# Kernel tuning notes

Measured on AMD Instinct MI355X. Metric: run time of the kernel, lower is better.

The kernel has to match this reference:

```python
import jax, jax.numpy as jnp
import numpy as np

N = 50000   # nodes
E = 800000  # edges
IN, H, OUT = 64, 512, 128


def _lin_init(key, out_dim, in_dim):
    kw, kb = jax.random.split(key)
    bound = 1.0 / np.sqrt(in_dim)
    W = jax.random.uniform(kw, (out_dim, in_dim), jnp.float32, -bound, bound)
    b = jax.random.uniform(kb, (out_dim,), jnp.float32, -bound, bound)
    return W, b


def setup_inputs() -> dict:
    key = jax.random.key(0)
    ks = jax.random.split(key, 10)
    x = jax.random.normal(ks[0], (N, IN), jnp.float32)
    edge_index = jax.random.randint(ks[1], (2, E), 0, N, jnp.int64)
    W_s1, b_s1 = _lin_init(ks[2], H, IN)
    W_s2, b_s2 = _lin_init(ks[3], H, H)
    W_s3, b_s3 = _lin_init(ks[4], H, H)
    W_s4, b_s4 = _lin_init(ks[5], H, H)
    W_m1, b_m1 = _lin_init(ks[6], OUT, H)
    W_m2, b_m2 = _lin_init(ks[7], OUT, OUT)
    W_l1, b_l1 = _lin_init(ks[8], OUT, H)
    W_l2, b_l2 = _lin_init(ks[9], OUT, OUT)
    return {"x": x, "edge_index": edge_index,
            "W_s1": W_s1, "b_s1": b_s1, "W_s2": W_s2, "b_s2": b_s2,
            "W_s3": W_s3, "b_s3": b_s3, "W_s4": W_s4, "b_s4": b_s4,
            "W_m1": W_m1, "b_m1": b_m1, "W_m2": W_m2, "b_m2": b_m2,
            "W_l1": W_l1, "b_l1": b_l1, "W_l2": W_l2, "b_l2": b_l2}


def _aggregate(h, src, dst):
    # GINConv with default eps=0: (1+eps)*x + sum_{j in N(i)} x_j
    return h + jax.ops.segment_sum(h[src], dst, num_segments=N)


def reference(x, edge_index,
              W_s1, b_s1, W_s2, b_s2, W_s3, b_s3, W_s4, b_s4,
              W_m1, b_m1, W_m2, b_m2, W_l1, b_l1, W_l2, b_l2):
    src, dst = edge_index[0], edge_index[1]
    lrelu = lambda v: jax.nn.leaky_relu(v, 0.1)

    def mlp_shared(h):
        h = lrelu(h @ W_s1.T + b_s1)
        h = lrelu(h @ W_s2.T + b_s2)
        h = lrelu(h @ W_s3.T + b_s3)
        return h @ W_s4.T + b_s4

    def mlp_mu(h):
        return jax.nn.relu(h @ W_m1.T + b_m1) @ W_m2.T + b_m2

    def mlp_logvar(h):
        return jax.nn.relu(h @ W_l1.T + b_l1) @ W_l2.T + b_l2

    h = jax.nn.relu(mlp_shared(_aggregate(x, src, dst)))
    mu = mlp_mu(_aggregate(h, src, dst))
    logvar = mlp_logvar(_aggregate(h, src, dst))
    return (mu, logvar)
```

## Files before the change

kernel.cpp:

```cpp
#include <hip/hip_runtime.h>
#include <hip/hip_bf16.h>
#include <stdint.h>

#define N_NODES 50000
#define N_PAD   50048
#define E_EDGES 800000
#define MT      391

typedef __bf16 bf16x8 __attribute__((ext_vector_type(8)));
typedef __bf16 bf16x4 __attribute__((ext_vector_type(4)));
typedef float  f32x4  __attribute__((ext_vector_type(4)));

__global__ void count_deg(const int* __restrict__ ei, int* __restrict__ cnt) {
    int e = blockIdx.x * blockDim.x + threadIdx.x;
    if (e < E_EDGES) atomicAdd(&cnt[ei[E_EDGES + e]], 1);
}

#define SCAN_B 1024
__global__ void scan_block(const int* __restrict__ cnt, int* __restrict__ ptr,
                           int* __restrict__ bsum, int n) {
    __shared__ int buf[SCAN_B];
    int i = blockIdx.x * SCAN_B + threadIdx.x;
    int v = (i < n) ? cnt[i] : 0;
    buf[threadIdx.x] = v;
    __syncthreads();
    #pragma unroll
    for (int off = 1; off < SCAN_B; off <<= 1) {
        int t = (threadIdx.x >= (unsigned)off) ? buf[threadIdx.x - off] : 0;
        __syncthreads();
        buf[threadIdx.x] += t;
        __syncthreads();
    }
    if (i < n) ptr[i] = buf[threadIdx.x] - v;
    if (threadIdx.x == SCAN_B - 1) bsum[blockIdx.x] = buf[SCAN_B - 1];
}

__global__ void scan_bsums(const int* __restrict__ bsum, int* __restrict__ boff,
                           int nb, int* __restrict__ total_out) {
    __shared__ int buf[SCAN_B];
    int v = ((int)threadIdx.x < nb) ? bsum[threadIdx.x] : 0;
    buf[threadIdx.x] = v;
    __syncthreads();
    #pragma unroll
    for (int off = 1; off < SCAN_B; off <<= 1) {
        int t = (threadIdx.x >= (unsigned)off) ? buf[threadIdx.x - off] : 0;
        __syncthreads();
        buf[threadIdx.x] += t;
        __syncthreads();
    }
    if ((int)threadIdx.x < nb) boff[threadIdx.x] = buf[threadIdx.x] - v;
    if (threadIdx.x == SCAN_B - 1) *total_out = buf[SCAN_B - 1];
}

__global__ void scan_add(int* __restrict__ ptr, const int* __restrict__ boff, int n) {
    int i = blockIdx.x * SCAN_B + threadIdx.x;
    if (i < n) ptr[i] += boff[blockIdx.x];
}

__global__ void fill_csr(const int* __restrict__ ei, const int* __restrict__ ptr,
                         int* __restrict__ cursor, int* __restrict__ col) {
    int e = blockIdx.x * blockDim.x + threadIdx.x;
    if (e < E_EDGES) {
        int dst = ei[E_EDGES + e];
        int pos = ptr[dst] + atomicAdd(&cursor[dst], 1);
        col[pos] = ei[e];
    }
}

#define XN      3200000
#define WTOT    983040
__global__ void cvt_all(const float* __restrict__ x,
                        const float* __restrict__ Ws1, const float* __restrict__ Ws2,
                        const float* __restrict__ Ws3, const float* __restrict__ Ws4,
                        const float* __restrict__ Wm1, const float* __restrict__ Wl1,
                        const float* __restrict__ Wm2, const float* __restrict__ Wl2,
                        __bf16* __restrict__ xb, __bf16* __restrict__ wbuf) {
    int i = blockIdx.x * blockDim.x + threadIdx.x;
    if (i < XN) { xb[i] = (__bf16)x[i]; return; }
    int j = i - XN;
    if (j >= WTOT) return;
    const float* s; int o;
    if      (j <  32768) { s = Ws1; o = j; }
    else if (j < 294912) { s = Ws2; o = j -  32768; }
    else if (j < 557056) { s = Ws3; o = j - 294912; }
    else if (j < 819200) { s = Ws4; o = j - 557056; }
    else if (j < 884736) { s = Wm1; o = j - 819200; }
    else if (j < 950272) { s = Wl1; o = j - 884736; }
    else if (j < 966656) { s = Wm2; o = j - 950272; }
    else                 { s = Wl2; o = j - 966656; }
    wbuf[j] = (__bf16)s[o];
}

__global__ __launch_bounds__(256) void agg0_gather(
    const __bf16* __restrict__ xb, const int* __restrict__ ptr,
    const int* __restrict__ col, __bf16* __restrict__ out) {
    int node = blockIdx.x * 4 + (threadIdx.x >> 6);
    int lane = threadIdx.x & 63;
    int g    = lane >> 3;
    int f0   = (lane & 7) << 3;
    if (node >= N_PAD) return;
    long o = (long)node * 64 + f0;
    if (node >= N_NODES) {
        if (g == 0) {
            bf16x8 z;
            #pragma unroll
            for (int i = 0; i < 8; ++i) z[i] = (__bf16)0.0f;
            *(bf16x8*)&out[o] = z;
        }
        return;
    }
    float a[8];
    #pragma unroll
    for (int i = 0; i < 8; ++i) a[i] = 0.0f;
    if (g == 0) {
        bf16x8 s = *(const bf16x8*)&xb[o];
        #pragma unroll
        for (int i = 0; i < 8; ++i) a[i] = (float)s[i];
    }
    int e0 = ptr[node], e1 = ptr[node + 1];
    int e = e0;
    for (; e + 16 <= e1; e += 16) {
        int c0 = col[e + g];
        int c1 = col[e + 8 + g];
        bf16x8 v0 = *(const bf16x8*)&xb[(c0 << 6) + f0];
        bf16x8 v1 = *(const bf16x8*)&xb[(c1 << 6) + f0];
        #pragma unroll
        for (int i = 0; i < 8; ++i) a[i] += (float)v0[i] + (float)v1[i];
    }
    int rem = e1 - e;
    if (rem > 0) {
        int u0 = (g < rem) ? g : 0;        float m0 = (g < rem) ? 1.0f : 0.0f;
        int i1 = g + 8;
        int u1 = (i1 < rem) ? i1 : 0;      float m1 = (i1 < rem) ? 1.0f : 0.0f;
        int c0 = col[e + u0];
        int c1 = col[e + u1];
        bf16x8 v0 = *(const bf16x8*)&xb[(c0 << 6) + f0];
        bf16x8 v1 = *(const bf16x8*)&xb[(c1 << 6) + f0];
        #pragma unroll
        for (int i = 0; i < 8; ++i) a[i] += m0 * (float)v0[i] + m1 * (float)v1[i];
    }
    #pragma unroll
    for (int i = 0; i < 8; ++i) {
        a[i] += __shfl_xor(a[i], 8, 64);
        a[i] += __shfl_xor(a[i], 16, 64);
        a[i] += __shfl_xor(a[i], 32, 64);
    }
    if (g == 0) {
        bf16x8 r;
        #pragma unroll
        for (int i = 0; i < 8; ++i) r[i] = (__bf16)a[i];
        *(bf16x8*)&out[o] = r;
    }
}

__global__ __launch_bounds__(256) void aggt_gather(
    const __bf16* __restrict__ t, const int* __restrict__ ptr,
    const int* __restrict__ col, const float* __restrict__ b_m1,
    const float* __restrict__ b_l1, __bf16* __restrict__ p) {
    int node = blockIdx.x * 8 + (threadIdx.x >> 5);
    if (node >= N_NODES) return;
    int hl = threadIdx.x & 31;
    int f0 = hl << 3;
    float a[8];
    {
        bf16x8 s = *(const bf16x8*)&t[((long)node << 8) + f0];
        #pragma unroll
        for (int i = 0; i < 8; ++i) a[i] = (float)s[i];
    }
    int e0 = ptr[node], e1 = ptr[node + 1];
    int e = e0;
    for (; e + 8 <= e1; e += 8) {
        int c[8];
        #pragma unroll
        for (int u = 0; u < 8; ++u) c[u] = col[e + u];
        bf16x8 v[8];
        #pragma unroll
        for (int u = 0; u < 8; ++u) v[u] = *(const bf16x8*)&t[((long)c[u] << 8) + f0];
        #pragma unroll
        for (int u = 0; u < 8; ++u)
            #pragma unroll
            for (int i = 0; i < 8; ++i) a[i] += (float)v[u][i];
    }
    int rem = e1 - e;
    if (rem > 0) {
        #pragma unroll
        for (int u = 0; u < 7; ++u) {
            int   uu = (u < rem) ? u : 0;
            float m  = (u < rem) ? 1.0f : 0.0f;
            int   cc = col[e + uu];
            bf16x8 v = *(const bf16x8*)&t[((long)cc << 8) + f0];
            #pragma unroll
            for (int i = 0; i < 8; ++i) a[i] += m * (float)v[i];
        }
    }
    const float* bp = (f0 < 128) ? (b_m1 + f0) : (b_l1 + (f0 - 128));
    f32x4 b0 = *(const f32x4*)bp;
    f32x4 b1 = *(const f32x4*)(bp + 4);
    bf16x8 r;
    #pragma unroll
    for (int i = 0; i < 4; ++i) r[i]     = (__bf16)fmaxf(a[i]     + b0[i], 0.0f);
    #pragma unroll
    for (int i = 0; i < 4; ++i) r[4 + i] = (__bf16)fmaxf(a[4 + i] + b1[i], 0.0f);
    *(bf16x8*)&p[((long)node << 8) + f0] = r;
}

__device__ __forceinline__ void gl_lds16(const __bf16* g, __bf16* l) {
    __builtin_amdgcn_global_load_lds(
        (const __attribute__((address_space(1))) uint32_t*)g,
        (__attribute__((address_space(3))) uint32_t*)l, 16, 0, 0);
}

#define P_WAITN(n) asm volatile("s_waitcnt vmcnt(" #n ")" ::: "memory")
#define P_LGKM0 asm volatile("s_waitcnt lgkmcnt(0)" ::: "memory")
#define P_BAR   __builtin_amdgcn_s_barrier()

__device__ __forceinline__ void stage_chunk(const __bf16* __restrict__ W, int Kdim,
                                            int k0, bool rows512,
                                            __bf16* __restrict__ buf,
                                            int wid, int lane) {
    if (rows512) {
        int r16 = lane >> 2, sl = lane & 3;
        #pragma unroll
        for (int i = 0; i < 4; ++i) {
            int cc = wid * 4 + i;
            int r  = cc * 16 + r16;
            int kt = sl ^ ((r >> 1) & 3);
            gl_lds16(W + (long)r * Kdim + k0 + kt * 8, buf + cc * 512);
        }
    } else {
        int r8 = lane >> 3, sl = lane & 7;
        #pragma unroll
        for (int i = 0; i < 4; ++i) {
            int cc = wid * 4 + i;
            int r  = cc * 8 + r8;
            int kt = sl ^ (r & 7);
            gl_lds16(W + (long)r * Kdim + k0 + kt * 8, buf + cc * 512);
        }
    }
}

__device__ __forceinline__ void chunk_mfma4(const __bf16* __restrict__ sAct,
    const __bf16* __restrict__ buf, int c, int rA, int q, int wncol,
    f32x4 (&acc)[4][4]) {
    const int g   = c * 4 + q;
    const int sla = ((g & 56) | ((g & 7) ^ (rA & 7))) << 3;
    bf16x8 af[4], bfr[4];
    #pragma unroll
    for (int mi = 0; mi < 4; ++mi)
        af[mi] = *(const bf16x8*)&sAct[(mi * 16 + rA) * 512 + sla];
    #pragma unroll
    for (int ni = 0; ni < 4; ++ni) {
        int wr = wncol + ni * 16 + rA;
        bfr[ni] = *(const bf16x8*)&buf[wr * 32 + ((q ^ ((wr >> 1) & 3)) << 3)];
    }
    #pragma unroll
    for (int mi = 0; mi < 4; ++mi)
        #pragma unroll
        for (int ni = 0; ni < 4; ++ni)
            acc[mi][ni] = __builtin_amdgcn_mfma_f32_16x16x32_bf16(
                af[mi], bfr[ni], acc[mi][ni], 0, 0, 0);
}

__device__ __forceinline__ void chunk_mfma_a0(const __bf16* __restrict__ act0,
    const __bf16* __restrict__ buf, int c, int rA, int q, int wncol,
    f32x4 (&acc)[4][4]) {
    const int g   = c * 4 + q;
    const int sla = (g ^ (rA & 7)) << 3;
    bf16x8 af[4], bfr[4];
    #pragma unroll
    for (int mi = 0; mi < 4; ++mi)
        af[mi] = *(const bf16x8*)&act0[(mi * 16 + rA) * 64 + sla];
    #pragma unroll
    for (int ni = 0; ni < 4; ++ni) {
        int wr = wncol + ni * 16 + rA;
        bfr[ni] = *(const bf16x8*)&buf[wr * 32 + ((q ^ ((wr >> 1) & 3)) << 3)];
    }
    #pragma unroll
    for (int mi = 0; mi < 4; ++mi)
        #pragma unroll
        for (int ni = 0; ni < 4; ++ni)
            acc[mi][ni] = __builtin_amdgcn_mfma_f32_16x16x32_bf16(
                af[mi], bfr[ni], acc[mi][ni], 0, 0, 0);
}

__device__ __forceinline__ void chunk_mfma_proj(const __bf16* __restrict__ sAct,
    const __bf16* __restrict__ buf, int c, int rA, int q, int wnp,
    f32x4 (&accp)[4][2]) {
    #pragma unroll
    for (int s = 0; s < 2; ++s) {
        const int g   = c * 8 + s * 4 + q;
        const int sla = ((g & 56) | ((g & 7) ^ (rA & 7))) << 3;
        bf16x8 af[4], bfr[2];
        #pragma unroll
        for (int mi = 0; mi < 4; ++mi)
            af[mi] = *(const bf16x8*)&sAct[(mi * 16 + rA) * 512 + sla];
        #pragma unroll
        for (int ni = 0; ni < 2; ++ni) {
            int wr = wnp + ni * 16 + rA;
            int gB = s * 4 + q;
            bfr[ni] = *(const bf16x8*)&buf[wr * 64 + ((gB ^ (wr & 7)) << 3)];
        }
        #pragma unroll
        for (int mi = 0; mi < 4; ++mi)
            #pragma unroll
            for (int ni = 0; ni < 2; ++ni)
                accp[mi][ni] = __builtin_amdgcn_mfma_f32_16x16x32_bf16(
                    af[mi], bfr[ni], accp[mi][ni], 0, 0, 0);
    }
}

template <int ACTn>
__device__ __forceinline__ void writeback_act(__bf16* __restrict__ sAct,
    f32x4 (&acc)[4][4], const float* __restrict__ bv,
    int wn, int ccol, int crow) {
    #pragma unroll
    for (int mi = 0; mi < 4; ++mi)
        #pragma unroll
        for (int ni = 0; ni < 4; ++ni) {
            int cc = wn + ni * 16 + ccol;
            int g  = cc >> 3;
            #pragma unroll
            for (int p = 0; p < 4; ++p) {
                int rr = mi * 16 + crow + p;
                float v = acc[mi][ni][p] + bv[ni];
                if (ACTn == 1) v = (v > 0.0f) ? v : 0.1f * v;
                else           v = fmaxf(v, 0.0f);
                int sl = (g & 56) | ((g & 7) ^ (rr & 7));
                sAct[rr * 512 + sl * 8 + (cc & 7)] = (__bf16)v;
            }
        }
}

template <int ACTn>
__device__ __forceinline__ void layer512_pipe(
    __bf16* __restrict__ sAct, __bf16* __restrict__ s0, __bf16* __restrict__ s1,
    const __bf16* __restrict__ W,
    const __bf16* __restrict__ Wn, int Kn, bool n512, int k0n_c1,
    const float* __restrict__ bv,
    int wn, int rA, int q, int ccol, int crow, int wid, int lane) {
    f32x4 acc[4][4];
    #pragma unroll
    for (int i = 0; i < 4; ++i)
        #pragma unroll
        for (int j = 0; j < 4; ++j) acc[i][j] = (f32x4)0.0f;
    #pragma unroll
    for (int c = 0; c < 16; ++c) {
        __bf16* cur = (c & 1) ? s1 : s0;
        P_WAITN(4); P_BAR;
        chunk_mfma4(sAct, cur, c, rA, q, wn, acc);
        if (c < 15) {
            P_LGKM0; P_BAR;
            if (c <= 13) stage_chunk(W, 512, (c + 2) * 32, true, cur, wid, lane);
            else         stage_chunk(Wn, Kn, 0, n512, s0, wid, lane);
        } else {
            P_LGKM0; P_BAR;
            writeback_act<ACTn>(sAct, acc, bv, wn, ccol, crow);
            __syncthreads();
            stage_chunk(Wn, Kn, k0n_c1, n512, s1, wid, lane);
        }
    }
}

__global__ __launch_bounds__(512) void mlp_fused(
    const __bf16* __restrict__ a0,
    const __bf16* __restrict__ w1, const float* __restrict__ b1,
    const __bf16* __restrict__ w2, const float* __restrict__ b2,
    const __bf16* __restrict__ w3, const float* __restrict__ b3,
    const __bf16* __restrict__ w4, const float* __restrict__ b4,
    const __bf16* __restrict__ wp,
    __bf16* __restrict__ tg)
{
    __shared__ __bf16 lds[69632];
    __bf16* act0 = lds;
    __bf16* sAct = lds + 4096;
    __bf16* s0   = lds + 36864;
    __bf16* s1   = lds + 53248;

    const int tid  = threadIdx.x;
    const int wid  = tid >> 6;
    const int lane = tid & 63;
    const long blockRow = (long)blockIdx.x * 64;

    const int rA   = lane & 15;
    const int q    = lane >> 4;
    const int ccol = lane & 15;
    const int crow = (lane >> 4) << 2;
    const int wn   = wid << 6;
    const int wnp  = wid << 5;

    float bv1[4], bv2[4], bv3[4], bv4[4];
    #pragma unroll
    for (int ni = 0; ni < 4; ++ni) {
        int idx = wn + ni * 16 + ccol;
        bv1[ni] = b1[idx]; bv2[ni] = b2[idx]; bv3[ni] = b3[idx]; bv4[ni] = b4[idx];
    }

    {
        int srow = lane >> 3;
        int skg  = (lane & 7) ^ srow;
        gl_lds16(a0 + (blockRow + wid * 8 + srow) * 64 + skg * 8, act0 + wid * 512);
    }
    stage_chunk(w1, 64, 0,  true, s0, wid, lane);
    stage_chunk(w1, 64, 32, true, s1, wid, lane);

    {
        f32x4 acc[4][4];
        #pragma unroll
        for (int i = 0; i < 4; ++i)
            #pragma unroll
            for (int j = 0; j < 4; ++j) acc[i][j] = (f32x4)0.0f;
        P_WAITN(4); P_BAR;
        chunk_mfma_a0(act0, s0, 0, rA, q, wn, acc);
        P_LGKM0; P_BAR;
        stage_chunk(w2, 512, 0, true, s0, wid, lane);
        P_WAITN(4); P_BAR;
        chunk_mfma_a0(act0, s1, 1, rA, q, wn, acc);
        writeback_act<1>(sAct, acc, bv1, wn, ccol, crow);
        __syncthreads();
        stage_chunk(w2, 512, 32, true, s1, wid, lane);
    }

    layer512_pipe<1>(sAct, s0, s1, w2, w3, 512, true, 32, bv2, wn, rA, q, ccol, crow, wid, lane);
    layer512_pipe<1>(sAct, s0, s1, w3, w4, 512, true, 32, bv3, wn, rA, q, ccol, crow, wid, lane);
    layer512_pipe<2>(sAct, s0, s1, w4, wp, 512, false, 64, bv4, wn, rA, q, ccol, crow, wid, lane);

    {
        f32x4 accp[4][2];
        #pragma unroll
        for (int i = 0; i < 4; ++i)
            #pragma unroll
            for (int j = 0; j < 2; ++j) accp[i][j] = (f32x4)0.0f;
        #pragma unroll
        for (int c = 0; c < 8; ++c) {
            __bf16* cur = (c & 1) ? s1 : s0;
            if (c == 7) { P_WAITN(0); } else { P_WAITN(4); }
            P_BAR;
            chunk_mfma_proj(sAct, cur, c, rA, q, wnp, accp);
            P_LGKM0; P_BAR;
            if (c < 6) stage_chunk(wp, 512, (c + 2) * 64, false, cur, wid, lane);
        }
        #pragma unroll
        for (int mi = 0; mi < 4; ++mi)
            #pragma unroll
            for (int ni = 0; ni < 2; ++ni)
                #pragma unroll
                for (int p = 0; p < 4; ++p)
                    s0[(mi * 16 + crow + p) * 256 + wnp + ni * 16 + ccol] =
                        (__bf16)accp[mi][ni][p];
        __syncthreads();
        int rr = tid >> 3;
        int c0 = (tid & 7) << 5;
        const bf16x8* s = (const bf16x8*)&s0[rr * 256 + c0];
        __bf16* d = tg + (blockRow + rr) * 256 + c0;
        #pragma unroll
        for (int i = 0; i < 4; ++i) *(bf16x8*)(d + i * 8) = s[i];
    }
}

template <int NCOL>
__device__ __forceinline__ void swizzle_xy(int bid, int& x, int& y) {
    int grp  = bid / (8 * NCOL);
    int rem  = bid - grp * (8 * NCOL);
    int base = grp * 8;
    int width = MT - base; if (width > 8) width = 8;
    x = base + rem % width;
    y = rem / width;
}

template <int ACT, bool BIAS, bool OUT_BF16, bool MCHK>
__device__ __forceinline__ void gemm_core(
    const __bf16* __restrict__ A, int lda, const __bf16* __restrict__ W,
    const float* __restrict__ bias, void* __restrict__ Cout, int ldc,
    int K, long Mstore, long blockRow, int blockCol,
    __bf16* __restrict__ smem) {
    __bf16* As = smem;
    __bf16* Ws = smem + 8192;
    const int tid  = threadIdx.x;
    const int wid  = tid >> 6;
    const int lane = tid & 63;
    const int wm = (wid >> 1) << 6;
    const int wn = (wid & 1) << 6;

    f32x4 acc[4][4];
    #pragma unroll
    for (int i = 0; i < 4; ++i)
        #pragma unroll
        for (int j = 0; j < 4; ++j) acc[i][j] = (f32x4)0.0f;

    const int srow = lane >> 3;
    const int skg  = (lane & 7) ^ srow;
    const __bf16* gA[4]; const __bf16* gW[4];
    __bf16 *lA[4], *lW[4];
    #pragma unroll
    for (int i = 0; i < 4; ++i) {
        int c = wid * 4 + i;
        gA[i] = A + (blockRow + c * 8 + srow) * (long)lda + skg * 8;
        gW[i] = W + ((long)blockCol + c * 8 + srow) * (long)K + skg * 8;
        lA[i] = As + c * 512;
        lW[i] = Ws + c * 512;
    }

    const int rA = lane & 15;
    const int q  = lane >> 4;
    const int r7 = rA & 7;

    for (int k0 = 0; k0 < K; k0 += 64) {
        #pragma unroll
        for (int i = 0; i < 4; ++i) gl_lds16(gA[i] + k0, lA[i]);
        #pragma unroll
        for (int i = 0; i < 4; ++i) gl_lds16(gW[i] + k0, lW[i]);
        __syncthreads();

        #pragma unroll
        for (int s = 0; s < 2; ++s) {
            const int slot = ((s * 4 + q) ^ r7) * 8;
            bf16x8 af[4], bf[4];
            #pragma unroll
            for (int mi = 0; mi < 4; ++mi)
                af[mi] = *(const bf16x8*)&As[(wm + mi * 16 + rA) * 64 + slot];
            #pragma unroll
            for (int ni = 0; ni < 4; ++ni)
                bf[ni] = *(const bf16x8*)&Ws[(wn + ni * 16 + rA) * 64 + slot];
            #pragma unroll
            for (int mi = 0; mi < 4; ++mi)
                #pragma unroll
                for (int ni = 0; ni < 4; ++ni)
                    acc[mi][ni] = __builtin_amdgcn_mfma_f32_16x16x32_bf16(
                        af[mi], bf[ni], acc[mi][ni], 0, 0, 0);
        }
        __syncthreads();
    }

    const int ccol = lane & 15;
    const int crow = (lane >> 4) << 2;
    if (OUT_BF16 && !MCHK) {
        #pragma unroll
        for (int mi = 0; mi < 4; ++mi) {
            #pragma unroll
            for (int ni = 0; ni < 4; ++ni) {
                int gc = wn + ni * 16 + ccol;
                float bv = BIAS ? bias[blockCol + gc] : 0.0f;
                #pragma unroll
                for (int r = 0; r < 4; ++r) {
                    float v = acc[mi][ni][r] + bv;
                    if (ACT == 1) v = (v > 0.0f) ? v : 0.1f * v;
                    else if (ACT == 2) v = fmaxf(v, 0.0f);
                    smem[(wm + mi * 16 + crow + r) * 128 + gc] = (__bf16)v;
                }
            }
        }
        __syncthreads();
        #pragma unroll
        for (int i = 0; i < 8; ++i) {
            int o   = (i * 256 + tid) * 8;
            int row = o >> 7;
            int co  = o & 127;
            *(bf16x8*)((__bf16*)Cout + (blockRow + row) * (long)ldc + blockCol + co) =
                *(const bf16x8*)&smem[o];
        }
    } else if (!OUT_BF16) {
        float* fsmem = (float*)smem;
        #pragma unroll
        for (int half = 0; half < 2; ++half) {
            __syncthreads();
            if ((wm >> 6) == half) {
                #pragma unroll
                for (int mi = 0; mi < 4; ++mi) {
                    #pragma unroll
                    for (int ni = 0; ni < 4; ++ni) {
                        int gc = wn + ni * 16 + ccol;
                        float bv = BIAS ? bias[blockCol + gc] : 0.0f;
                        #pragma unroll
                        for (int r = 0; r < 4; ++r) {
                            float v = acc[mi][ni][r] + bv;
                            if (ACT == 1) v = (v > 0.0f) ? v : 0.1f * v;
                            else if (ACT == 2) v = fmaxf(v, 0.0f);
                            fsmem[(mi * 16 + crow + r) * 128 + gc] = v;
                        }
                    }
                }
            }
            __syncthreads();
            #pragma unroll
            for (int i = 0; i < 8; ++i) {
                int o   = i * 256 + tid;
                int row = o >> 5;
                int co  = (o & 31) * 4;
                long gr = blockRow + half * 64 + row;
                if (!MCHK || gr < Mstore)
                    *(f32x4*)((float*)Cout + gr * (long)ldc + blockCol + co) =
                        *(const f32x4*)&fsmem[o * 4];
            }
        }
    } else {
        #pragma unroll
        for (int mi = 0; mi < 4; ++mi) {
            #pragma unroll
            for (int ni = 0; ni < 4; ++ni) {
                long gr0 = blockRow + wm + mi * 16 + crow;
                int  gc  = blockCol + wn + ni * 16 + ccol;
                float bv = BIAS ? bias[gc] : 0.0f;
                #pragma unroll
                for (int r = 0; r < 4; ++r) {
                    long gr = gr0 + r;
                    if (!MCHK || gr < Mstore) {
                        float v = acc[mi][ni][r] + bv;
                        if (ACT == 1) v = (v > 0.0f) ? v : 0.1f * v;
                        else if (ACT == 2) v = fmaxf(v, 0.0f);
                        ((__bf16*)Cout)[gr * ldc + gc] = (__bf16)v;
                    }
                }
            }
        }
    }
}

__global__ __launch_bounds__(256) void gemm_heads(
    const __bf16* __restrict__ p, const __bf16* __restrict__ wm2,
    const float* __restrict__ b_m2, float* __restrict__ mu,
    const __bf16* __restrict__ wl2, const float* __restrict__ b_l2,
    float* __restrict__ lv) {
    __shared__ __bf16 smem[128 * 128];
    int x, hd;
    swizzle_xy<2>(blockIdx.x, x, hd);
    if (hd == 0)
        gemm_core<0, true, false, true>(p, 256, wm2, b_m2, mu, 128, 128, N_NODES,
                                        (long)x * 128, 0, smem);
    else
        gemm_core<0, true, false, true>(p + 128, 256, wl2, b_l2, lv, 128, 128, N_NODES,
                                        (long)x * 128, 0, smem);
}

extern "C" void kernel_launch(void* const* d_in, const int* in_sizes, int n_in,
                              void* d_out, int out_size, void* d_ws, size_t ws_size,
                              hipStream_t stream) {
    const float* x    = (const float*)d_in[0];
    const int*   ei   = (const int*)d_in[1];
    const float* W_s1 = (const float*)d_in[2];
    const float* b_s1 = (const float*)d_in[3];
    const float* W_s2 = (const float*)d_in[4];
    const float* b_s2 = (const float*)d_in[5];
    const float* W_s3 = (const float*)d_in[6];
    const float* b_s3 = (const float*)d_in[7];
    const float* W_s4 = (const float*)d_in[8];
    const float* b_s4 = (const float*)d_in[9];
    const float* W_m1 = (const float*)d_in[10];
    const float* b_m1 = (const float*)d_in[11];
    const float* W_m2 = (const float*)d_in[12];
    const float* b_m2 = (const float*)d_in[13];
    const float* W_l1 = (const float*)d_in[14];
    const float* b_l1 = (const float*)d_in[15];
    const float* W_l2 = (const float*)d_in[16];
    const float* b_l2 = (const float*)d_in[17];

    char* ws = (char*)d_ws;
    size_t off = 0;
    auto carve = [&](size_t bytes) -> void* {
        void* p = ws + off;
        off = (off + bytes + 255) & ~(size_t)255;
        return p;
    };
    int* ptr  = (int*)carve((size_t)(N_NODES + 1) * 4);
    int* col  = (int*)carve((size_t)E_EDGES * 4);
    int* bsum = (int*)carve(SCAN_B * 4);
    int* boff = (int*)carve(SCAN_B * 4);
    __bf16* wbuf = (__bf16*)carve((size_t)WTOT * 2);
    __bf16* w1  = wbuf;
    __bf16* w2  = wbuf +  32768;
    __bf16* w3  = wbuf + 294912;
    __bf16* w4  = wbuf + 557056;
    __bf16* wml = wbuf + 819200;
    __bf16* wm2 = wbuf + 950272;
    __bf16* wl2 = wbuf + 966656;
    __bf16* xb    = (__bf16*)carve((size_t)XN * 2);
    __bf16* agg0b = (__bf16*)carve((size_t)N_PAD * 64 * 2);
    __bf16* B1    = (__bf16*)carve((size_t)N_PAD * 512 * 2);
    __bf16* B2    = (__bf16*)carve((size_t)N_PAD * 512 * 2);

    int* cnt = (int*)B1;
    int* cur = (int*)B2;

    (void)hipMemsetAsync(cnt, 0, (size_t)N_NODES * 4, stream);
    (void)hipMemsetAsync(cur, 0, (size_t)N_NODES * 4, stream);

    const int NB = (N_NODES + SCAN_B - 1) / SCAN_B;
    count_deg<<<E_EDGES / 256, 256, 0, stream>>>(ei, cnt);
    scan_block<<<NB, SCAN_B, 0, stream>>>(cnt, ptr, bsum, N_NODES);
    scan_bsums<<<1, SCAN_B, 0, stream>>>(bsum, boff, NB, &ptr[N_NODES]);
    scan_add<<<NB, SCAN_B, 0, stream>>>(ptr, boff, N_NODES);
    fill_csr<<<E_EDGES / 256, 256, 0, stream>>>(ei, ptr, cur, col);

    cvt_all<<<(XN + WTOT + 255) / 256, 256, 0, stream>>>(
        x, W_s1, W_s2, W_s3, W_s4, W_m1, W_l1, W_m2, W_l2, xb, wbuf);

    agg0_gather<<<N_PAD / 4, 256, 0, stream>>>(xb, ptr, col, agg0b);

    __bf16* t = B1;
    mlp_fused<<<N_PAD / 64, 512, 0, stream>>>(agg0b, w1, b_s1, w2, b_s2,
                                              w3, b_s3, w4, b_s4, wml, t);

    __bf16* p = B2;
    aggt_gather<<<(N_NODES + 7) / 8, 256, 0, stream>>>(t, ptr, col, b_m1, b_l1, p);

    float* mu = (float*)d_out;
    float* lv = mu + (size_t)N_NODES * 128;
    gemm_heads<<<MT * 2, 256, 0, stream>>>(p, wm2, b_m2, mu, wl2, b_l2, lv);
}
```

Before: 442.4 us.

## Triple-buffer weight chunks to drop per-chunk barrier and raise MFMA priority

Replaces the double-buffered weight staging in the fused MLP kernel with a three-slot ring buffer. Each chunk's global-to-LDS load is issued before the MFMAs for the current chunk, which removes the second barrier and the lgkmcnt wait per chunk and lets loads overlap compute. It also wraps the MFMA blocks in s_setprio to favour matrix issue. LDS use rises from about 136KB to 160KB per block, and the wait counts and slot rotation across layers must line up exactly or results will be wrong.

```diff
diff --git a/kernel.cpp b/kernel.cpp
--- a/kernel.cpp
+++ b/kernel.cpp
@@ -211,8 +211,10 @@
 }
 
 #define P_WAITN(n) asm volatile("s_waitcnt vmcnt(" #n ")" ::: "memory")
-#define P_LGKM0 asm volatile("s_waitcnt lgkmcnt(0)" ::: "memory")
-#define P_BAR   __builtin_amdgcn_s_barrier()
+#define P_WAIT0    asm volatile("s_waitcnt vmcnt(0)" ::: "memory")
+#define P_LGKM0    asm volatile("s_waitcnt lgkmcnt(0)" ::: "memory")
+#define P_BAR      __builtin_amdgcn_s_barrier()
+#define SLOT_ELEMS 16384
 
 __device__ __forceinline__ void stage_chunk(const __bf16* __restrict__ W, int Kdim,
                                             int k0, bool rows512,
@@ -253,12 +255,14 @@
         int wr = wncol + ni * 16 + rA;
         bfr[ni] = *(const bf16x8*)&buf[wr * 32 + ((q ^ ((wr >> 1) & 3)) << 3)];
     }
+    __builtin_amdgcn_s_setprio(1);
     #pragma unroll
     for (int mi = 0; mi < 4; ++mi)
         #pragma unroll
         for (int ni = 0; ni < 4; ++ni)
             acc[mi][ni] = __builtin_amdgcn_mfma_f32_16x16x32_bf16(
                 af[mi], bfr[ni], acc[mi][ni], 0, 0, 0);
+    __builtin_amdgcn_s_setprio(0);
 }
 
 __device__ __forceinline__ void chunk_mfma_a0(const __bf16* __restrict__ act0,
@@ -275,17 +279,20 @@
         int wr = wncol + ni * 16 + rA;
         bfr[ni] = *(const bf16x8*)&buf[wr * 32 + ((q ^ ((wr >> 1) & 3)) << 3)];
     }
+    __builtin_amdgcn_s_setprio(1);
     #pragma unroll
     for (int mi = 0; mi < 4; ++mi)
         #pragma unroll
         for (int ni = 0; ni < 4; ++ni)
             acc[mi][ni] = __builtin_amdgcn_mfma_f32_16x16x32_bf16(
                 af[mi], bfr[ni], acc[mi][ni], 0, 0, 0);
+    __builtin_amdgcn_s_setprio(0);
 }
 
 __device__ __forceinline__ void chunk_mfma_proj(const __bf16* __restrict__ sAct,
     const __bf16* __restrict__ buf, int c, int rA, int q, int wnp,
     f32x4 (&accp)[4][2]) {
+    __builtin_amdgcn_s_setprio(1);
     #pragma unroll
     for (int s = 0; s < 2; ++s) {
         const int g   = c * 8 + s * 4 + q;
@@ -307,6 +314,7 @@
                 accp[mi][ni] = __builtin_amdgcn_mfma_f32_16x16x32_bf16(
                     af[mi], bfr[ni], accp[mi][ni], 0, 0, 0);
     }
+    __builtin_amdgcn_s_setprio(0);
 }
 
 template <int ACTn>
@@ -331,11 +339,11 @@
         }
 }
 
-template <int ACTn>
-__device__ __forceinline__ void layer512_pipe(
-    __bf16* __restrict__ sAct, __bf16* __restrict__ s0, __bf16* __restrict__ s1,
+template <int ACTn, int B3>
+__device__ __forceinline__ void layer512_pipe3(
+    __bf16* __restrict__ sAct, __bf16* __restrict__ sbase,
     const __bf16* __restrict__ W,
-    const __bf16* __restrict__ Wn, int Kn, bool n512, int k0n_c1,
+    const __bf16* __restrict__ Wn, int Kn, bool n512, int k0n_c0, int k0n_c1,
     const float* __restrict__ bv,
     int wn, int rA, int q, int ccol, int crow, int wid, int lane) {
     f32x4 acc[4][4];
@@ -345,20 +353,16 @@
         for (int j = 0; j < 4; ++j) acc[i][j] = (f32x4)0.0f;
     #pragma unroll
     for (int c = 0; c < 16; ++c) {
-        __bf16* cur = (c & 1) ? s1 : s0;
         P_WAITN(4); P_BAR;
-        chunk_mfma4(sAct, cur, c, rA, q, wn, acc);
-        if (c < 15) {
-            P_LGKM0; P_BAR;
-            if (c <= 13) stage_chunk(W, 512, (c + 2) * 32, true, cur, wid, lane);
-            else         stage_chunk(Wn, Kn, 0, n512, s0, wid, lane);
-        } else {
-            P_LGKM0; P_BAR;
-            writeback_act<ACTn>(sAct, acc, bv, wn, ccol, crow);
-            __syncthreads();
-            stage_chunk(Wn, Kn, k0n_c1, n512, s1, wid, lane);
-        }
-    }
+        __bf16* dst = sbase + (((B3 + c + 2) % 3) * SLOT_ELEMS);
+        if (c <= 13)      stage_chunk(W, 512, (c + 2) * 32, true, dst, wid, lane);
+        else if (c == 14) stage_chunk(Wn, Kn, k0n_c0, n512, dst, wid, lane);
+        else              stage_chunk(Wn, Kn, k0n_c1, n512, dst, wid, lane);
+        chunk_mfma4(sAct, sbase + (((B3 + c) % 3) * SLOT_ELEMS), c, rA, q, wn, acc);
+    }
+    P_BAR;
+    writeback_act<ACTn>(sAct, acc, bv, wn, ccol, crow);
+    P_LGKM0; P_BAR;
 }
 
 __global__ __launch_bounds__(512) void mlp_fused(
@@ -370,11 +374,9 @@
     const __bf16* __restrict__ wp,
     __bf16* __restrict__ tg)
 {
-    __shared__ __bf16 lds[69632];
-    __bf16* act0 = lds;
-    __bf16* sAct = lds + 4096;
-    __bf16* s0   = lds + 36864;
-    __bf16* s1   = lds + 53248;
+    __shared__ __bf16 lds[81920];
+    __bf16* sAct  = lds;
+    __bf16* sbase = lds + 32768;
 
     const int tid  = threadIdx.x;
     const int wid  = tid >> 6;
@@ -398,10 +400,10 @@
     {
         int srow = lane >> 3;
         int skg  = (lane & 7) ^ srow;
-        gl_lds16(a0 + (blockRow + wid * 8 + srow) * 64 + skg * 8, act0 + wid * 512);
-    }
-    stage_chunk(w1, 64, 0,  true, s0, wid, lane);
-    stage_chunk(w1, 64, 32, true, s1, wid, lane);
+        gl_lds16(a0 + (blockRow + wid * 8 + srow) * 64 + skg * 8, lds + wid * 512);
+    }
+    stage_chunk(w1, 64, 0,  true, sbase,              wid, lane);
+    stage_chunk(w1, 64, 32, true, sbase + SLOT_ELEMS, wid, lane);
 
     {
         f32x4 acc[4][4];
@@ -409,20 +411,23 @@
         for (int i = 0; i < 4; ++i)
             #pragma unroll
             for (int j = 0; j < 4; ++j) acc[i][j] = (f32x4)0.0f;
+        P_WAIT0; P_BAR;
+        stage_chunk(w2, 512, 0, true, sbase + 2 * SLOT_ELEMS, wid, lane);
+        chunk_mfma_a0(lds, sbase, 0, rA, q, wn, acc);
         P_WAITN(4); P_BAR;
-        chunk_mfma_a0(act0, s0, 0, rA, q, wn, acc);
+        stage_chunk(w2, 512, 32, true, sbase, wid, lane);
+        chunk_mfma_a0(lds, sbase + SLOT_ELEMS, 1, rA, q, wn, acc);
+        P_BAR;
+        writeback_act<1>(sAct, acc, bv1, wn, ccol, crow);
         P_LGKM0; P_BAR;
-        stage_chunk(w2, 512, 0, true, s0, wid, lane);
-        P_WAITN(4); P_BAR;
-        chunk_mfma_a0(act0, s1, 1, rA, q, wn, acc);
-        writeback_act<1>(sAct, acc, bv1, wn, ccol, crow);
-        __syncthreads();
-        stage_chunk(w2, 512, 32, true, s1, wid, lane);
-    }
-
-    layer512_pipe<1>(sAct, s0, s1, w2, w3, 512, true, 32, bv2, wn, rA, q, ccol, crow, wid, lane);
-    layer512_pipe<1>(sAct, s0, s1, w3, w4, 512, true, 32, bv3, wn, rA, q, ccol, crow, wid, lane);
-    layer512_pipe<2>(sAct, s0, s1, w4, wp, 512, false, 64, bv4, wn, rA, q, ccol, crow, wid, lane);
+    }
+
+    layer512_pipe3<1, 2>(sAct, sbase, w2, w3, 512, true, 0, 32, bv2,
+                         wn, rA, q, ccol, crow, wid, lane);
+    layer512_pipe3<1, 0>(sAct, sbase, w3, w4, 512, true, 0, 32, bv3,
+                         wn, rA, q, ccol, crow, wid, lane);
+    layer512_pipe3<2, 1>(sAct, sbase, w4, wp, 512, false, 0, 64, bv4,
+                         wn, rA, q, ccol, crow, wid, lane);
 
     {
         f32x4 accp[4][2];
@@ -432,13 +437,16 @@
             for (int j = 0; j < 2; ++j) accp[i][j] = (f32x4)0.0f;
         #pragma unroll
         for (int c = 0; c < 8; ++c) {
-            __bf16* cur = (c & 1) ? s1 : s0;
-            if (c == 7) { P_WAITN(0); } else { P_WAITN(4); }
+            if (c == 7) { P_WAIT0; } else { P_WAITN(4); }
             P_BAR;
-            chunk_mfma_proj(sAct, cur, c, rA, q, wnp, accp);
-            P_LGKM0; P_BAR;
-            if (c < 6) stage_chunk(wp, 512, (c + 2) * 64, false, cur, wid, lane);
-        }
+            if (c <= 5)
+                stage_chunk(wp, 512, (c + 2) * 64, false,
+                            sbase + (((4 + c) % 3) * SLOT_ELEMS), wid, lane);
+            chunk_mfma_proj(sAct, sbase + (((2 + c) % 3) * SLOT_ELEMS),
+                            c, rA, q, wnp, accp);
+        }
+        P_BAR;
+        __bf16* s0 = sbase;
         #pragma unroll
         for (int mi = 0; mi < 4; ++mi)
             #pragma unroll
```

New measurement: 443.4 us. About the same (+0.2%).

## Fuse first-layer neighbor aggregation into MLP kernel and merge degree count with conversion

Applied to the files above, without the earlier changes.

Moves the layer-0 GIN aggregation out of its own gather kernel and into the start of the fused MLP kernel. There, each thread sums one node's 8-feature slice over its neighbors and writes the result straight into swizzled LDS, so the intermediate agg0 buffer is no longer written and re-read. The degree-count atomics are folded into the dtype conversion kernel, which removes two launches overall. The trade-off is that the in-kernel gather uses one thread per node slice with sequential edge loops. That may give less memory-level parallelism than the old wave-wide gather and adds latency before the first MFMA chunk.

```diff
diff --git a/kernel.cpp b/kernel.cpp
--- a/kernel.cpp
+++ b/kernel.cpp
@@ -10,11 +10,6 @@
 typedef __bf16 bf16x8 __attribute__((ext_vector_type(8)));
 typedef __bf16 bf16x4 __attribute__((ext_vector_type(4)));
 typedef float  f32x4  __attribute__((ext_vector_type(4)));
-
-__global__ void count_deg(const int* __restrict__ ei, int* __restrict__ cnt) {
-    int e = blockIdx.x * blockDim.x + threadIdx.x;
-    if (e < E_EDGES) atomicAdd(&cnt[ei[E_EDGES + e]], 1);
-}
 
 #define SCAN_B 1024
 __global__ void scan_block(const int* __restrict__ cnt, int* __restrict__ ptr,
@@ -69,88 +64,32 @@
 
 #define XN      3200000
 #define WTOT    983040
-__global__ void cvt_all(const float* __restrict__ x,
-                        const float* __restrict__ Ws1, const float* __restrict__ Ws2,
-                        const float* __restrict__ Ws3, const float* __restrict__ Ws4,
-                        const float* __restrict__ Wm1, const float* __restrict__ Wl1,
-                        const float* __restrict__ Wm2, const float* __restrict__ Wl2,
-                        __bf16* __restrict__ xb, __bf16* __restrict__ wbuf) {
+__global__ void cvt_count(const float* __restrict__ x,
+                          const float* __restrict__ Ws1, const float* __restrict__ Ws2,
+                          const float* __restrict__ Ws3, const float* __restrict__ Ws4,
+                          const float* __restrict__ Wm1, const float* __restrict__ Wl1,
+                          const float* __restrict__ Wm2, const float* __restrict__ Wl2,
+                          const int* __restrict__ ei,
+                          __bf16* __restrict__ xb, __bf16* __restrict__ wbuf,
+                          int* __restrict__ cnt) {
     int i = blockIdx.x * blockDim.x + threadIdx.x;
     if (i < XN) { xb[i] = (__bf16)x[i]; return; }
     int j = i - XN;
-    if (j >= WTOT) return;
-    const float* s; int o;
-    if      (j <  32768) { s = Ws1; o = j; }
-    else if (j < 294912) { s = Ws2; o = j -  32768; }
-    else if (j < 557056) { s = Ws3; o = j - 294912; }
-    else if (j < 819200) { s = Ws4; o = j - 557056; }
-    else if (j < 884736) { s = Wm1; o = j - 819200; }
-    else if (j < 950272) { s = Wl1; o = j - 884736; }
-    else if (j < 966656) { s = Wm2; o = j - 950272; }
-    else                 { s = Wl2; o = j - 966656; }
-    wbuf[j] = (__bf16)s[o];
-}
-
-__global__ __launch_bounds__(256) void agg0_gather(
-    const __bf16* __restrict__ xb, const int* __restrict__ ptr,
-    const int* __restrict__ col, __bf16* __restrict__ out) {
-    int node = blockIdx.x * 4 + (threadIdx.x >> 6);
-    int lane = threadIdx.x & 63;
-    int g    = lane >> 3;
-    int f0   = (lane & 7) << 3;
-    if (node >= N_PAD) return;
-    long o = (long)node * 64 + f0;
-    if (node >= N_NODES) {
-        if (g == 0) {
-            bf16x8 z;
-            #pragma unroll
-            for (int i = 0; i < 8; ++i) z[i] = (__bf16)0.0f;
-            *(bf16x8*)&out[o] = z;
-        }
+    if (j < WTOT) {
+        const float* s; int o;
+        if      (j <  32768) { s = Ws1; o = j; }
+        else if (j < 294912) { s = Ws2; o = j -  32768; }
+        else if (j < 557056) { s = Ws3; o = j - 294912; }
+        else if (j < 819200) { s = Ws4; o = j - 557056; }
+        else if (j < 884736) { s = Wm1; o = j - 819200; }
+        else if (j < 950272) { s = Wl1; o = j - 884736; }
+        else if (j < 966656) { s = Wm2; o = j - 950272; }
+        else                 { s = Wl2; o = j - 966656; }
+        wbuf[j] = (__bf16)s[o];
         return;
     }
-    float a[8];
-    #pragma unroll
-    for (int i = 0; i < 8; ++i) a[i] = 0.0f;
-    if (g == 0) {
-        bf16x8 s = *(const bf16x8*)&xb[o];
-        #pragma unroll
-        for (int i = 0; i < 8; ++i) a[i] = (float)s[i];
-    }
-    int e0 = ptr[node], e1 = ptr[node + 1];
-    int e = e0;
-    for (; e + 16 <= e1; e += 16) {
-        int c0 = col[e + g];
-        int c1 = col[e + 8 + g];
-        bf16x8 v0 = *(const bf16x8*)&xb[(c0 << 6) + f0];
-        bf16x8 v1 = *(const bf16x8*)&xb[(c1 << 6) + f0];
-        #pragma unroll
-        for (int i = 0; i < 8; ++i) a[i] += (float)v0[i] + (float)v1[i];
-    }
-    int rem = e1 - e;
-    if (rem > 0) {
-        int u0 = (g < rem) ? g : 0;        float m0 = (g < rem) ? 1.0f : 0.0f;
-        int i1 = g + 8;
-        int u1 = (i1 < rem) ? i1 : 0;      float m1 = (i1 < rem) ? 1.0f : 0.0f;
-        int c0 = col[e + u0];
-        int c1 = col[e + u1];
-        bf16x8 v0 = *(const bf16x8*)&xb[(c0 << 6) + f0];
-        bf16x8 v1 = *(const bf16x8*)&xb[(c1 << 6) + f0];
-        #pragma unroll
-        for (int i = 0; i < 8; ++i) a[i] += m0 * (float)v0[i] + m1 * (float)v1[i];
-    }
-    #pragma unroll
-    for (int i = 0; i < 8; ++i) {
-        a[i] += __shfl_xor(a[i], 8, 64);
-        a[i] += __shfl_xor(a[i], 16, 64);
-        a[i] += __shfl_xor(a[i], 32, 64);
-    }
-    if (g == 0) {
-        bf16x8 r;
-        #pragma unroll
-        for (int i = 0; i < 8; ++i) r[i] = (__bf16)a[i];
-        *(bf16x8*)&out[o] = r;
-    }
+    int e = j - WTOT;
+    if (e < E_EDGES) atomicAdd(&cnt[ei[E_EDGES + e]], 1);
 }
 
 __global__ __launch_bounds__(256) void aggt_gather(
@@ -211,8 +150,9 @@
 }
 
 #define P_WAITN(n) asm volatile("s_waitcnt vmcnt(" #n ")" ::: "memory")
-#define P_LGKM0 asm volatile("s_waitcnt lgkmcnt(0)" ::: "memory")
-#define P_BAR   __builtin_amdgcn_s_barrier()
+#define P_WAIT0    asm volatile("s_waitcnt vmcnt(0)" ::: "memory")
+#define P_LGKM0    asm volatile("s_waitcnt lgkmcnt(0)" ::: "memory")
+#define P_BAR      __builtin_amdgcn_s_barrier()
 
 __device__ __forceinline__ void stage_chunk(const __bf16* __restrict__ W, int Kdim,
                                             int k0, bool rows512,
@@ -362,7 +302,8 @@
 }
 
 __global__ __launch_bounds__(512) void mlp_fused(
-    const __bf16* __restrict__ a0,
+    const __bf16* __restrict__ xb,
+    const int* __restrict__ ptr, const int* __restrict__ col,
     const __bf16* __restrict__ w1, const float* __restrict__ b1,
     const __bf16* __restrict__ w2, const float* __restrict__ b2,
     const __bf16* __restrict__ w3, const float* __restrict__ b3,
@@ -388,6 +329,9 @@
     const int wn   = wid << 6;
     const int wnp  = wid << 5;
 
+    stage_chunk(w1, 64, 0,  true, s0, wid, lane);
+    stage_chunk(w1, 64, 32, true, s1, wid, lane);
+
     float bv1[4], bv2[4], bv3[4], bv4[4];
     #pragma unroll
     for (int ni = 0; ni < 4; ++ni) {
@@ -396,12 +340,44 @@
     }
 
     {
-        int srow = lane >> 3;
-        int skg  = (lane & 7) ^ srow;
-        gl_lds16(a0 + (blockRow + wid * 8 + srow) * 64 + skg * 8, act0 + wid * 512);
-    }
-    stage_chunk(w1, 64, 0,  true, s0, wid, lane);
-    stage_chunk(w1, 64, 32, true, s1, wid, lane);
+        int nl = tid >> 3;
+        int fj = tid & 7;
+        long gnode = blockRow + nl;
+        float a[8];
+        #pragma unroll
+        for (int i = 0; i < 8; ++i) a[i] = 0.0f;
+        if (gnode < N_NODES) {
+            bf16x8 s = *(const bf16x8*)&xb[gnode * 64 + fj * 8];
+            #pragma unroll
+            for (int i = 0; i < 8; ++i) a[i] = (float)s[i];
+            int e0 = ptr[gnode], e1 = ptr[gnode + 1];
+            int e = e0;
+            for (; e + 4 <= e1; e += 4) {
+                int c0 = col[e], c1 = col[e + 1], c2 = col[e + 2], c3 = col[e + 3];
+                bf16x8 v0 = *(const bf16x8*)&xb[((long)c0 << 6) + fj * 8];
+                bf16x8 v1 = *(const bf16x8*)&xb[((long)c1 << 6) + fj * 8];
+                bf16x8 v2 = *(const bf16x8*)&xb[((long)c2 << 6) + fj * 8];
+                bf16x8 v3 = *(const bf16x8*)&xb[((long)c3 << 6) + fj * 8];
+                #pragma unroll
+                for (int i = 0; i < 8; ++i)
+                    a[i] += ((float)v0[i] + (float)v1[i]) +
+                            ((float)v2[i] + (float)v3[i]);
+            }
+            for (; e < e1; ++e) {
+                bf16x8 v = *(const bf16x8*)&xb[((long)col[e] << 6) + fj * 8];
+                #pragma unroll
+                for (int i = 0; i < 8; ++i) a[i] += (float)v[i];
+            }
+        }
+        bf16x8 r;
+        #pragma unroll
+        for (int i = 0; i < 8; ++i) r[i] = (__bf16)a[i];
+        int slot = fj ^ (nl & 7);
+        *(bf16x8*)&act0[nl * 64 + slot * 8] = r;
+    }
+
+    asm volatile("s_waitcnt vmcnt(0) lgkmcnt(0)" ::: "memory");
+    P_BAR;
 
     {
         f32x4 acc[4][4];
@@ -409,7 +385,6 @@
         for (int i = 0; i < 4; ++i)
             #pragma unroll
             for (int j = 0; j < 4; ++j) acc[i][j] = (f32x4)0.0f;
-        P_WAITN(4); P_BAR;
         chunk_mfma_a0(act0, s0, 0, rA, q, wn, acc);
         P_LGKM0; P_BAR;
         stage_chunk(w2, 512, 0, true, s0, wid, lane);
@@ -433,7 +408,7 @@
         #pragma unroll
         for (int c = 0; c < 8; ++c) {
             __bf16* cur = (c & 1) ? s1 : s0;
-            if (c == 7) { P_WAITN(0); } else { P_WAITN(4); }
+            if (c == 7) { P_WAIT0; } else { P_WAITN(4); }
             P_BAR;
             chunk_mfma_proj(sAct, cur, c, rA, q, wnp, accp);
             P_LGKM0; P_BAR;
@@ -673,7 +648,6 @@
     __bf16* wm2 = wbuf + 950272;
     __bf16* wl2 = wbuf + 966656;
     __bf16* xb    = (__bf16*)carve((size_t)XN * 2);
-    __bf16* agg0b = (__bf16*)carve((size_t)N_PAD * 64 * 2);
     __bf16* B1    = (__bf16*)carve((size_t)N_PAD * 512 * 2);
     __bf16* B2    = (__bf16*)carve((size_t)N_PAD * 512 * 2);
 
@@ -683,20 +657,17 @@
     (void)hipMemsetAsync(cnt, 0, (size_t)N_NODES * 4, stream);
     (void)hipMemsetAsync(cur, 0, (size_t)N_NODES * 4, stream);
 
+    cvt_count<<<(XN + WTOT + E_EDGES + 255) / 256, 256, 0, stream>>>(
+        x, W_s1, W_s2, W_s3, W_s4, W_m1, W_l1, W_m2, W_l2, ei, xb, wbuf, cnt);
+
     const int NB = (N_NODES + SCAN_B - 1) / SCAN_B;
-    count_deg<<<E_EDGES / 256, 256, 0, stream>>>(ei, cnt);
     scan_block<<<NB, SCAN_B, 0, stream>>>(cnt, ptr, bsum, N_NODES);
     scan_bsums<<<1, SCAN_B, 0, stream>>>(bsum, boff, NB, &ptr[N_NODES]);
     scan_add<<<NB, SCAN_B, 0, stream>>>(ptr, boff, N_NODES);
     fill_csr<<<E_EDGES / 256, 256, 0, stream>>>(ei, ptr, cur, col);
 
-    cvt_all<<<(XN + WTOT + 255) / 256, 256, 0, stream>>>(
-        x, W_s1, W_s2, W_s3, W_s4, W_m1, W_l1, W_m2, W_l2, xb, wbuf);
-
-    agg0_gather<<<N_PAD / 4, 256, 0, stream>>>(xb, ptr, col, agg0b);
-
     __bf16* t = B1;
-    mlp_fused<<<N_PAD / 64, 512, 0, stream>>>(agg0b, w1, b_s1, w2, b_s2,
+    mlp_fused<<<N_PAD / 64, 512, 0, stream>>>(xb, ptr, col, w1, b_s1, w2, b_s2,
                                               w3, b_s3, w4, b_s4, wml, t);
 
     __bf16* p = B2;
```

New measurement: 457.8 us. 1.03x slower.
